# Performance work log

Hardware: AMD Instinct MI355X
Metric: run time of the kernel (lower is better)

## Reference

```python
import jax, jax.numpy as jnp
import numpy as np
import math

B, S, D, H, FF = 2, 2048, 1024, 16, 4096
E = D // H  # per-head dim = 64
LN_EPS = 1e-5


def _layernorm(x, g, b):
    m = jnp.mean(x, axis=-1, keepdims=True)
    v = jnp.var(x, axis=-1, keepdims=True)
    return (x - m) * jax.lax.rsqrt(v + LN_EPS) * g + b


def setup_inputs() -> dict:
    key = jax.random.key(0)
    ks = jax.random.split(key, 12)
    std = 0.02
    return {
        "inputs": jax.random.normal(ks[0], (B, S, D), dtype=jnp.float32),
        "ln1_g": jnp.ones((D,), jnp.float32),
        "ln1_b": jnp.zeros((D,), jnp.float32),
        # per-head q/k/v Linear(D, E) stacked along head axis: [H, D, E]
        "wq": jax.random.normal(ks[1], (H, D, E), jnp.float32) * std,
        "bq": jax.random.normal(ks[2], (H, E), jnp.float32) * std,
        "wk": jax.random.normal(ks[3], (H, D, E), jnp.float32) * std,
        "bk": jax.random.normal(ks[4], (H, E), jnp.float32) * std,
        "wv": jax.random.normal(ks[5], (H, D, E), jnp.float32) * std,
        "bv": jax.random.normal(ks[6], (H, E), jnp.float32) * std,
        "wo": jax.random.normal(ks[7], (D, D), jnp.float32) * std,
        "bo": jnp.zeros((D,), jnp.float32),
        "ln2_g": jnp.ones((D,), jnp.float32),
        "ln2_b": jnp.zeros((D,), jnp.float32),
        "w1": jax.random.normal(ks[8], (D, FF), jnp.float32) * std,
        "b1": jnp.zeros((FF,), jnp.float32),
        "w2": jax.random.normal(ks[9], (FF, D), jnp.float32) * std,
        "b2": jnp.zeros((D,), jnp.float32),
    }


def reference(inputs, ln1_g, ln1_b, wq, bq, wk, bk, wv, bv, wo, bo,
              ln2_g, ln2_b, w1, b1, w2, b2):
    d_model = inputs.shape[-1]
    scale = jnp.asarray(math.sqrt(d_model), inputs.dtype)  # NOTE: sqrt(d_model), not d_head

    x1 = _layernorm(inputs, ln1_g, ln1_b)
    # batched per-head projections (original uses H separate Linear layers)
    q = jnp.einsum('bsd,hde->bhse', x1, wq) + bq[None, :, None, :]
    k = jnp.einsum('bsd,hde->bhse', x1, wk) + bk[None, :, None, :]
    v = jnp.einsum('bsd,hde->bhse', x1, wv) + bv[None, :, None, :]

    scores = jnp.einsum('bhqe,bhke->bhqk', q, k) / scale
    # original: nn.Softmax(dim=1) on [B, S_q, S_k] -> softmax over the QUERY axis
    attn = jax.nn.softmax(scores, axis=2)
    a = jnp.einsum('bhqk,bhke->bhqe', attn, v)  # [B, H, S, E]

    # concat heads along feature dim (head 0 first)
    bsz, _, slen, _ = a.shape
    a = a.transpose(0, 2, 1, 3).reshape(bsz, slen, d_model)
    msa = a @ wo + bo

    inter = msa + inputs
    x2 = _layernorm(inter, ln2_g, ln2_b)
    mlp = jax.nn.gelu(x2 @ w1 + b1, approximate=False) @ w2 + b2
    return mlp + inter
```

## Files before the change

### kernel.cpp

```cpp
#include <hip/hip_runtime.h>
#include <hip/hip_bf16.h>

typedef unsigned short u16;
typedef __attribute__((ext_vector_type(8))) short short8;
typedef __attribute__((ext_vector_type(4))) float f32x4;
typedef __attribute__((ext_vector_type(4))) unsigned short us4;
typedef __attribute__((ext_vector_type(4))) float float4v;

#define DEV __device__ __forceinline__

DEV float b2f(u16 v){ return __uint_as_float(((unsigned)v)<<16); }
DEV u16 f2b(float f){
  unsigned u = __float_as_uint(f);
  u = u + 0x7FFFu + ((u>>16)&1u);
  return (u16)(u>>16);
}
DEV f32x4 mfma16(short8 a, short8 b, f32x4 c){
  return __builtin_amdgcn_mfma_f32_16x16x32_bf16(a, b, c, 0, 0, 0);
}
DEV void async16(const void* g, const void* l){
  __builtin_amdgcn_global_load_lds(
    (const __attribute__((address_space(1))) unsigned int*)(uintptr_t)g,
    (__attribute__((address_space(3))) unsigned int*)(unsigned int)(uintptr_t)l,
    16, 0, 0);
}

__global__ __launch_bounds__(256) void ln_k(const float* __restrict__ xin,
    const float* __restrict__ g, const float* __restrict__ bb, u16* __restrict__ y)
{
  const int row = blockIdx.x, t = threadIdx.x, l = t&63, w = t>>6;
  const float4v rr = *(const float4v*)(xin + (size_t)row*1024 + t*4);
  float v[4] = {rr[0], rr[1], rr[2], rr[3]};
  float s  = v[0]+v[1]+v[2]+v[3];
  float ss = v[0]*v[0]+v[1]*v[1]+v[2]*v[2]+v[3]*v[3];
#pragma unroll
  for (int off=32; off>=1; off>>=1){
    s  += __shfl_down(s,  off, 64);
    ss += __shfl_down(ss, off, 64);
  }
  __shared__ float rs[4], rq[4];
  if (l==0){ rs[w]=s; rq[w]=ss; }
  __syncthreads();
  const float S = rs[0]+rs[1]+rs[2]+rs[3];
  const float Q = rq[0]+rq[1]+rq[2]+rq[3];
  const float mean = S*(1.0f/1024.0f);
  const float var  = Q*(1.0f/1024.0f) - mean*mean;
  const float rstd = rsqrtf(var + 1e-5f);
  const float4v gg = *(const float4v*)(g  + t*4);
  const float4v bv = *(const float4v*)(bb + t*4);
  us4 o;
#pragma unroll
  for (int j=0;j<4;j++) o[j] = f2b((v[j]-mean)*rstd*gg[j] + bv[j]);
  *(us4*)(y + (size_t)row*1024 + t*4) = o;
}

__global__ void transpose_k(const float* __restrict__ src, u16* __restrict__ dst,
                            int ldsrc, int lddst)
{
  __shared__ u16 tile[32][33];
  const int tx = threadIdx.x & 31, ty = threadIdx.x >> 5;
  const int c0 = blockIdx.x*32, r0 = blockIdx.y*32;
#pragma unroll
  for (int i=0;i<32;i+=8) tile[ty+i][tx] = f2b(src[(size_t)(r0+ty+i)*ldsrc + c0+tx]);
  __syncthreads();
#pragma unroll
  for (int i=0;i<32;i+=8) dst[(size_t)(c0+ty+i)*lddst + r0+tx] = tile[tx][ty+i];
}

__global__ void pack_qkv_k(const float* __restrict__ wq, const float* __restrict__ wk,
                           const float* __restrict__ wv, u16* __restrict__ BT)
{
  __shared__ u16 tile[32][33];
  const int z = blockIdx.z, which = z>>4, h = z&15;
  const float* w = (which==0?wq:(which==1?wk:wv)) + (size_t)h*1024*64;
  u16* d = BT + (size_t)(which*1024 + h*64)*1024;
  const int tx = threadIdx.x & 31, ty = threadIdx.x >> 5;
  const int c0 = blockIdx.x*32, r0 = blockIdx.y*32;
#pragma unroll
  for (int i=0;i<32;i+=8) tile[ty+i][tx] = f2b(w[(size_t)(r0+ty+i)*64 + c0+tx]);
  __syncthreads();
#pragma unroll
  for (int i=0;i<32;i+=8) d[(size_t)(c0+ty+i)*1024 + r0+tx] = tile[tx][ty+i];
}

__global__ void pack_bias_k(const float* __restrict__ bq, const float* __restrict__ bk,
                            const float* __restrict__ bv, float* __restrict__ dst)
{
  const int t = blockIdx.x*256 + threadIdx.x;
  const float* s = (t < 1024) ? bq : (t < 2048 ? bk : bv);
  dst[t] = s[t & 1023];
}

__global__ __launch_bounds__(256) void inv_l(const float* __restrict__ L, float* __restrict__ invL)
{
  const int i = blockIdx.x*256 + threadIdx.x;
  invL[i] = 1.0f / (L[i] + L[i + 65536]);
}

template<int EPI>
__global__ __launch_bounds__(256) void gemm_bt(
    const u16* __restrict__ A, const u16* __restrict__ BT,
    const float* __restrict__ bias, const float* __restrict__ resf,
    u16* __restrict__ outb, float* __restrict__ outf,
    int K, int lda, int ldb, int ldc)
{
  __shared__ u16 Asm[128*32];
  __shared__ u16 Bsm[128*32];
  const int t = threadIdx.x, l = t&63, w = t>>6;
  const int bn = blockIdx.x, bm = blockIdx.y;
  const u16* gA = A  + (size_t)(bm*128 + (t>>2))*lda + (t&3)*8;
  const u16* gB = BT + (size_t)(bn*128 + (t>>2))*ldb + (t&3)*8;
  char* lA = (char*)Asm + t*16;
  char* lB = (char*)Bsm + t*16;
  const int wr = (w>>1)*64, wc = (w&1)*64;
  f32x4 acc[4][4] = {};
  for (int kt = 0; kt < K; kt += 32) {
    __syncthreads();
    async16(gA + kt,                    lA);
    async16(gA + kt + (size_t)64*lda,   lA + 4096);
    async16(gB + kt,                    lB);
    async16(gB + kt + (size_t)64*ldb,   lB + 4096);
    __syncthreads();
    short8 af[4], bf[4];
#pragma unroll
    for (int m=0;m<4;m++) af[m] = *(const short8*)&Asm[(wr + m*16 + (l&15))*32 + (l>>4)*8];
#pragma unroll
    for (int n=0;n<4;n++) bf[n] = *(const short8*)&Bsm[(wc + n*16 + (l&15))*32 + (l>>4)*8];
#pragma unroll
    for (int m=0;m<4;m++)
#pragma unroll
      for (int n=0;n<4;n++)
        acc[m][n] = mfma16(af[m], bf[n], acc[m][n]);
  }
  const int rowb = bm*128 + wr, colb = bn*128 + wc;
#pragma unroll
  for (int m=0;m<4;m++)
#pragma unroll
    for (int n=0;n<4;n++){
      const int col = colb + n*16 + (l&15);
      const float bv = bias[col];
#pragma unroll
      for (int j=0;j<4;j++){
        const int row = rowb + m*16 + (l>>4)*4 + j;
        float v = acc[m][n][j] + bv;
        const size_t idx = (size_t)row*ldc + col;
        if constexpr (EPI==0)      outb[idx] = f2b(v);
        else if constexpr (EPI==1) outf[idx] = v + resf[idx];
        else                       outb[idx] = f2b(0.5f*v*(1.0f + erff(v*0.70710678118654752f)));
      }
    }
}

template<int EPI>
__global__ __launch_bounds__(256) void gemm_bt64(
    const u16* __restrict__ A, const u16* __restrict__ BT,
    const float* __restrict__ bias, const float* __restrict__ resf,
    u16* __restrict__ outb, float* __restrict__ outf,
    int K, int lda, int ldb, int ldc)
{
  __shared__ u16 Asm[128*32];
  __shared__ u16 Bsm[64*32];
  const int t = threadIdx.x, l = t&63, w = t>>6;
  const int bn = blockIdx.x, bm = blockIdx.y;
  const u16* gA = A  + (size_t)(bm*128 + (t>>2))*lda + (t&3)*8;
  const u16* gB = BT + (size_t)(bn*64  + (t>>2))*ldb + (t&3)*8;
  char* lA = (char*)Asm + t*16;
  char* lB = (char*)Bsm + t*16;
  const int wr = w*32;
  f32x4 acc[2][4] = {};
  for (int kt = 0; kt < K; kt += 32) {
    __syncthreads();
    async16(gA + kt,                    lA);
    async16(gA + kt + (size_t)64*lda,   lA + 4096);
    async16(gB + kt,                    lB);
    __syncthreads();
    short8 af[2], bf[4];
#pragma unroll
    for (int m=0;m<2;m++) af[m] = *(const short8*)&Asm[(wr + m*16 + (l&15))*32 + (l>>4)*8];
#pragma unroll
    for (int n=0;n<4;n++) bf[n] = *(const short8*)&Bsm[(n*16 + (l&15))*32 + (l>>4)*8];
#pragma unroll
    for (int m=0;m<2;m++)
#pragma unroll
      for (int n=0;n<4;n++)
        acc[m][n] = mfma16(af[m], bf[n], acc[m][n]);
  }
  const int rowb = bm*128 + wr, colb = bn*64;
#pragma unroll
  for (int m=0;m<2;m++)
#pragma unroll
    for (int n=0;n<4;n++){
      const int col = colb + n*16 + (l&15);
      const float bv = bias[col];
#pragma unroll
      for (int j=0;j<4;j++){
        const int row = rowb + m*16 + (l>>4)*4 + j;
        float v = acc[m][n][j] + bv;
        const size_t idx = (size_t)row*ldc + col;
        if constexpr (EPI==0)      outb[idx] = f2b(v);
        else if constexpr (EPI==1) outf[idx] = v + resf[idx];
        else                       outb[idx] = f2b(0.5f*v*(1.0f + erff(v*0.70710678118654752f)));
      }
    }
}


__global__ __launch_bounds__(256) void attn_stats(const u16* __restrict__ QKV, float* __restrict__ L)
{
  const int g = blockIdx.x;
  const int xcd = g & 7, s_ = g >> 3;
  const int bh   = xcd*4 + (s_ & 3);
  const int kblk = (s_ >> 2) & 15;
  const int part = s_ >> 6;
  const int b = bh>>4, h = bh&15;
  const u16* Qb = QKV + (size_t)b*2048*3072 + h*64;
  const u16* Kb = Qb + 1024;
  __shared__ u16 Klds[128*64];
  __shared__ float red[4][128];
  const int t = threadIdx.x, l = t&63, w = t>>6;
#pragma unroll
  for (int i=0;i<8;i++){
    const int c = t + i*256, r = c>>4, ch = c&15;
    us4 v = *(const us4*)(Kb + (size_t)(kblk*128 + r)*3072 + ch*4);
    *(us4*)((char*)Klds + ((r*128 + ch*8) ^ ((r&7)<<4))) = v;
  }
  __syncthreads();
  short8 kf[8][2];
#pragma unroll
  for (int n=0;n<8;n++){
    const int r = n*16 + (l&15);
    const int sw = (r&7)<<4;
#pragma unroll
    for (int ks=0;ks<2;ks++)
      kf[n][ks] = *(const short8*)((char*)Klds + ((r*128 + ks*64 + (l>>4)*16) ^ sw));
  }
  float Lacc[8] = {0,0,0,0,0,0,0,0};
  short8 qf[2][2], qn[2][2];
  {
    const int qb = part*1024 + w*32;
#pragma unroll
    for (int m=0;m<2;m++)
#pragma unroll
      for (int ks=0;ks<2;ks++)
        qf[m][ks] = *(const short8*)(Qb + (size_t)(qb + m*16 + (l&15))*3072 + ks*32 + (l>>4)*8);
  }
  for (int qt = 0; qt < 8; qt++){
    if (qt < 7){
      const int qb = part*1024 + (qt+1)*128 + w*32;
#pragma unroll
      for (int m=0;m<2;m++)
#pragma unroll
        for (int ks=0;ks<2;ks++)
          qn[m][ks] = *(const short8*)(Qb + (size_t)(qb + m*16 + (l&15))*3072 + ks*32 + (l>>4)*8);
    }
#pragma unroll
    for (int m=0;m<2;m++)
#pragma unroll
      for (int n=0;n<8;n++){
        f32x4 s = {};
        s = mfma16(qf[m][0], kf[n][0], s);
        s = mfma16(qf[m][1], kf[n][1], s);
#pragma unroll
        for (int j=0;j<4;j++) Lacc[n] += __expf(s[j]*0.03125f);
      }
    if (qt < 7){
#pragma unroll
      for (int m=0;m<2;m++)
#pragma unroll
        for (int ks=0;ks<2;ks++) qf[m][ks] = qn[m][ks];
    }
  }
#pragma unroll
  for (int n=0;n<8;n++){
    Lacc[n] += __shfl_xor(Lacc[n], 16, 64);
    Lacc[n] += __shfl_xor(Lacc[n], 32, 64);
  }
  if (l < 16){
#pragma unroll
    for (int n=0;n<8;n++) red[w][n*16 + l] = Lacc[n];
  }
  __syncthreads();
  if (t < 128)
    L[(size_t)part*65536 + (size_t)bh*2048 + kblk*128 + t]
        = red[0][t]+red[1][t]+red[2][t]+red[3][t];
}

__global__ __launch_bounds__(256) void attn_pv(const u16* __restrict__ QKV,
    const float* __restrict__ invL, u16* __restrict__ Aout)
{
  const int g = blockIdx.x;
  const int xcd = g & 7, s_ = g >> 3;
  const int bh = xcd*4 + (s_ & 3);
  const int qblk = s_ >> 2;
  const int b = bh>>4, h = bh&15;
  const u16* Qb = QKV + (size_t)b*2048*3072 + h*64;
  const u16* Kb = Qb + 1024;
  const u16* Vb = Qb + 2048;
  const float* iL = invL + (size_t)bh*2048;
  __shared__ u16 Klds[64*64];
  __shared__ u16 VT[64*66];
  __shared__ u16 P[64*68];
  __shared__ float iLs[64];
  const int t = threadIdx.x, l = t&63, w = t>>6;
  short8 qf[2];
#pragma unroll
  for (int ks=0;ks<2;ks++)
    qf[ks] = *(const short8*)(Qb + (size_t)(qblk*64 + w*16 + (l&15))*3072 + ks*32 + (l>>4)*8);
  int rr[4], cc[4];
#pragma unroll
  for (int i=0;i<4;i++){ const int c = t + i*256; rr[i] = c>>4; cc[i] = c&15; }
  us4 kreg[4], vreg[4];
#pragma unroll
  for (int i=0;i<4;i++){
    kreg[i] = *(const us4*)(Kb + (size_t)rr[i]*3072 + cc[i]*4);
    vreg[i] = *(const us4*)(Vb + (size_t)rr[i]*3072 + cc[i]*4);
  }
  float ilreg = (t < 64) ? iL[t] : 0.0f;
  f32x4 acc[4] = {};
  for (int kt=0; kt<2048; kt+=64){
#pragma unroll
    for (int i=0;i<4;i++)
      *(us4*)((char*)Klds + ((rr[i]*128 + cc[i]*8) ^ ((rr[i]&7)<<4))) = kreg[i];
    if (t < 64) iLs[t] = ilreg;
    __syncthreads();
#pragma unroll
    for (int i=0;i<4;i++){
#pragma unroll
      for (int jj=0;jj<4;jj++) VT[(cc[i]*4+jj)*66 + rr[i]] = vreg[i][jj];
    }
    if (kt + 64 < 2048){
      const u16* Kn = Kb + (size_t)(kt+64)*3072;
      const u16* Vn = Vb + (size_t)(kt+64)*3072;
#pragma unroll
      for (int i=0;i<4;i++){
        kreg[i] = *(const us4*)(Kn + (size_t)rr[i]*3072 + cc[i]*4);
        vreg[i] = *(const us4*)(Vn + (size_t)rr[i]*3072 + cc[i]*4);
      }
      if (t < 64) ilreg = iL[kt + 64 + t];
    }
    float il[4];
#pragma unroll
    for (int n=0;n<4;n++) il[n] = iLs[n*16 + (l&15)];
#pragma unroll
    for (int n=0;n<4;n++){
      const int r = n*16 + (l&15);
      const int sw = (r&7)<<4;
      const short8 kf0 = *(const short8*)((char*)Klds + ((r*128 +      (l>>4)*16) ^ sw));
      const short8 kf1 = *(const short8*)((char*)Klds + ((r*128 + 64 + (l>>4)*16) ^ sw));
      f32x4 s = {};
      s = mfma16(qf[0], kf0, s);
      s = mfma16(qf[1], kf1, s);
      const int prow = w*16 + (l>>4)*4;
      const int pcol = n*16 + (l&15);
#pragma unroll
      for (int j=0;j<4;j++)
        P[(prow+j)*68 + pcol] = f2b(__expf(s[j]*0.03125f) * il[n]);
    }
    __syncthreads();
#pragma unroll
    for (int kk=0;kk<2;kk++){
      const short8 af = *(const short8*)&P[(w*16 + (l&15))*68 + kk*32 + (l>>4)*8];
#pragma unroll
      for (int n=0;n<4;n++){
        const short8 bf = *(const short8*)&VT[(n*16 + (l&15))*66 + kk*32 + (l>>4)*8];
        acc[n] = mfma16(af, bf, acc[n]);
      }
    }
  }
  const int rowb = b*2048 + qblk*64 + w*16;
  const int colb = h*64;
#pragma unroll
  for (int n=0;n<4;n++)
#pragma unroll
    for (int j=0;j<4;j++){
      const int row = rowb + (l>>4)*4 + j;
      const int col = colb + n*16 + (l&15);
      Aout[(size_t)row*1024 + col] = f2b(acc[n][j]);
    }
}

extern "C" void kernel_launch(void* const* d_in, const int* in_sizes, int n_in,
                              void* d_out, int out_size, void* d_ws, size_t ws_size,
                              hipStream_t stream)
{
  const float* x    = (const float*)d_in[0];
  const float* ln1g = (const float*)d_in[1];
  const float* ln1b = (const float*)d_in[2];
  const float* wq   = (const float*)d_in[3];
  const float* bq   = (const float*)d_in[4];
  const float* wk   = (const float*)d_in[5];
  const float* bk   = (const float*)d_in[6];
  const float* wv   = (const float*)d_in[7];
  const float* bv   = (const float*)d_in[8];
  const float* wo   = (const float*)d_in[9];
  const float* bo   = (const float*)d_in[10];
  const float* ln2g = (const float*)d_in[11];
  const float* ln2b = (const float*)d_in[12];
  const float* w1   = (const float*)d_in[13];
  const float* b1   = (const float*)d_in[14];
  const float* w2   = (const float*)d_in[15];
  const float* b2   = (const float*)d_in[16];
  float* out = (float*)d_out;

  char* ws = (char*)d_ws;
  u16*   x1      = (u16*)  (ws + 0);
  u16*   QKV     = (u16*)  (ws + 8388608);
  u16*   H1      = (u16*)  (ws + 8388608);
  float* Lbuf    = (float*)(ws + 41943040);
  u16*   Aout    = (u16*)  (ws + 42467328);
  u16*   packbuf = (u16*)  (ws + 50855936);
  float* inter   = (float*)(ws + 59244544);
  float* biasqkv = (float*)(ws + 76021760);
  float* invLb   = (float*)(ws + 76038144);
  u16*   x2 = x1;

  pack_bias_k<<<12, 256, 0, stream>>>(bq, bk, bv, biasqkv);

  ln_k<<<4096, 256, 0, stream>>>(x, ln1g, ln1b, x1);
  pack_qkv_k<<<dim3(2,32,48), 256, 0, stream>>>(wq, wk, wv, packbuf);
  gemm_bt<0><<<dim3(24,32), 256, 0, stream>>>(x1, packbuf, biasqkv,
      nullptr, QKV, nullptr, 1024, 1024, 1024, 3072);

  attn_stats<<<1024, 256, 0, stream>>>(QKV, Lbuf);
  inv_l<<<256, 256, 0, stream>>>(Lbuf, invLb);
  attn_pv  <<<1024, 256, 0, stream>>>(QKV, invLb, Aout);

  transpose_k<<<dim3(32,32), 256, 0, stream>>>(wo, packbuf, 1024, 1024);
  gemm_bt64<1><<<dim3(16,32), 256, 0, stream>>>(Aout, packbuf, bo,
      x, nullptr, inter, 1024, 1024, 1024, 1024);

  ln_k<<<4096, 256, 0, stream>>>(inter, ln2g, ln2b, x2);

  transpose_k<<<dim3(128,32), 256, 0, stream>>>(w1, packbuf, 4096, 1024);
  gemm_bt<2><<<dim3(32,32), 256, 0, stream>>>(x2, packbuf, b1,
      nullptr, H1, nullptr, 1024, 1024, 1024, 4096);

  transpose_k<<<dim3(32,128), 256, 0, stream>>>(w2, packbuf, 1024, 4096);
  gemm_bt64<1><<<dim3(16,32), 256, 0, stream>>>(H1, packbuf, b2,
      inter, nullptr, out, 4096, 4096, 4096, 1024);
}
```

Before: 476.9 us.

## Double-buffer GEMM LDS tiles with K=64 steps and XOR-swizzled layout

Replaces the two single-buffered GEMM kernels with one templated kernel. It double-buffers LDS so the next tile's global-to-LDS async loads overlap the current tile's MFMAs, doubles the K step to 64, and XOR-swizzles the LDS chunk layout to cut bank conflicts on fragment reads. The cost is twice the LDS per block (about 64KB for BN=128), which can reduce occupancy. There is also a reliance on the async loads finishing at the single barrier per iteration.

```diff
diff --git a/kernel.cpp b/kernel.cpp
--- a/kernel.cpp
+++ b/kernel.cpp
@@ -97,97 +97,81 @@
   invL[i] = 1.0f / (L[i] + L[i + 65536]);
 }
 
-template<int EPI>
-__global__ __launch_bounds__(256) void gemm_bt(
+template<int EPI, int BN>
+__global__ __launch_bounds__(256) void gemm2(
     const u16* __restrict__ A, const u16* __restrict__ BT,
     const float* __restrict__ bias, const float* __restrict__ resf,
     u16* __restrict__ outb, float* __restrict__ outf,
     int K, int lda, int ldb, int ldc)
 {
-  __shared__ u16 Asm[128*32];
-  __shared__ u16 Bsm[128*32];
+  constexpr int MF   = (BN==128) ? 4 : 2;
+  constexpr int BISS = BN/32;
+  __shared__ u16 smem[2][(128+BN)*64];
   const int t = threadIdx.x, l = t&63, w = t>>6;
   const int bn = blockIdx.x, bm = blockIdx.y;
-  const u16* gA = A  + (size_t)(bm*128 + (t>>2))*lda + (t&3)*8;
-  const u16* gB = BT + (size_t)(bn*128 + (t>>2))*ldb + (t&3)*8;
-  char* lA = (char*)Asm + t*16;
-  char* lB = (char*)Bsm + t*16;
-  const int wr = (w>>1)*64, wc = (w&1)*64;
-  f32x4 acc[4][4] = {};
-  for (int kt = 0; kt < K; kt += 32) {
+  const int wr = (BN==128) ? (w>>1)*64 : w*32;
+  const int wc = (BN==128) ? (w&1)*64  : 0;
+  const int srow = t>>3;
+  const int schunk = ((t&7) ^ (srow&7)) * 8;
+  const u16* gA = A  + (size_t)(bm*128 + srow)*lda + schunk;
+  const u16* gB = BT + (size_t)(bn*BN  + srow)*ldb + schunk;
+  char* ldsA0 = (char*)&smem[0][0];
+  char* ldsB0 = (char*)&smem[0][128*64];
+  char* ldsA1 = (char*)&smem[1][0];
+  char* ldsB1 = (char*)&smem[1][128*64];
+  int colx[2];
+#pragma unroll
+  for (int kk=0;kk<2;kk++) colx[kk] = (kk*64 + (l>>4)*16) ^ ((l&7)<<4);
+  int rowA[MF], rowB[4];
+#pragma unroll
+  for (int m=0;m<MF;m++) rowA[m] = (wr + m*16 + (l&15))*128;
+#pragma unroll
+  for (int n=0;n<4;n++)  rowB[n] = (wc + n*16 + (l&15))*128;
+
+#define STAGE(bufA, bufB, kt)                                            \
+  {                                                                      \
+    _Pragma("unroll")                                                    \
+    for (int i=0;i<4;i++)                                                \
+      async16(gA + (kt) + (size_t)i*32*lda, (bufA) + i*4096 + t*16);     \
+    _Pragma("unroll")                                                    \
+    for (int i=0;i<BISS;i++)                                             \
+      async16(gB + (kt) + (size_t)i*32*ldb, (bufB) + i*4096 + t*16);     \
+  }
+
+  f32x4 acc[MF][4] = {};
+  STAGE(ldsA0, ldsB0, 0);
+  __syncthreads();
+  const int nt = K >> 6;
+  int cur = 0;
+  for (int ti = 0; ti < nt; ++ti){
+    char* cA = cur ? ldsA1 : ldsA0;
+    char* cB = cur ? ldsB1 : ldsB0;
+    if (ti + 1 < nt){
+      char* pA = cur ? ldsA0 : ldsA1;
+      char* pB = cur ? ldsB0 : ldsB1;
+      STAGE(pA, pB, (ti+1)*64);
+    }
+#pragma unroll
+    for (int kk=0;kk<2;kk++){
+      short8 af[MF], bf[4];
+#pragma unroll
+      for (int m=0;m<MF;m++) af[m] = *(const short8*)(cA + rowA[m] + colx[kk]);
+#pragma unroll
+      for (int n=0;n<4;n++)  bf[n] = *(const short8*)(cB + rowB[n] + colx[kk]);
+#pragma unroll
+      for (int m=0;m<MF;m++)
+#pragma unroll
+        for (int n=0;n<4;n++)
+          acc[m][n] = mfma16(af[m], bf[n], acc[m][n]);
+    }
     __syncthreads();
-    async16(gA + kt,                    lA);
-    async16(gA + kt + (size_t)64*lda,   lA + 4096);
-    async16(gB + kt,                    lB);
-    async16(gB + kt + (size_t)64*ldb,   lB + 4096);
-    __syncthreads();
-    short8 af[4], bf[4];
-#pragma unroll
-    for (int m=0;m<4;m++) af[m] = *(const short8*)&Asm[(wr + m*16 + (l&15))*32 + (l>>4)*8];
-#pragma unroll
-    for (int n=0;n<4;n++) bf[n] = *(const short8*)&Bsm[(wc + n*16 + (l&15))*32 + (l>>4)*8];
-#pragma unroll
-    for (int m=0;m<4;m++)
-#pragma unroll
-      for (int n=0;n<4;n++)
-        acc[m][n] = mfma16(af[m], bf[n], acc[m][n]);
-  }
-  const int rowb = bm*128 + wr, colb = bn*128 + wc;
-#pragma unroll
-  for (int m=0;m<4;m++)
-#pragma unroll
-    for (int n=0;n<4;n++){
-      const int col = colb + n*16 + (l&15);
-      const float bv = bias[col];
-#pragma unroll
-      for (int j=0;j<4;j++){
-        const int row = rowb + m*16 + (l>>4)*4 + j;
-        float v = acc[m][n][j] + bv;
-        const size_t idx = (size_t)row*ldc + col;
-        if constexpr (EPI==0)      outb[idx] = f2b(v);
-        else if constexpr (EPI==1) outf[idx] = v + resf[idx];
-        else                       outb[idx] = f2b(0.5f*v*(1.0f + erff(v*0.70710678118654752f)));
-      }
-    }
-}
-
-template<int EPI>
-__global__ __launch_bounds__(256) void gemm_bt64(
-    const u16* __restrict__ A, const u16* __restrict__ BT,
-    const float* __restrict__ bias, const float* __restrict__ resf,
-    u16* __restrict__ outb, float* __restrict__ outf,
-    int K, int lda, int ldb, int ldc)
-{
-  __shared__ u16 Asm[128*32];
-  __shared__ u16 Bsm[64*32];
-  const int t = threadIdx.x, l = t&63, w = t>>6;
-  const int bn = blockIdx.x, bm = blockIdx.y;
-  const u16* gA = A  + (size_t)(bm*128 + (t>>2))*lda + (t&3)*8;
-  const u16* gB = BT + (size_t)(bn*64  + (t>>2))*ldb + (t&3)*8;
-  char* lA = (char*)Asm + t*16;
-  char* lB = (char*)Bsm + t*16;
-  const int wr = w*32;
-  f32x4 acc[2][4] = {};
-  for (int kt = 0; kt < K; kt += 32) {
-    __syncthreads();
-    async16(gA + kt,                    lA);
-    async16(gA + kt + (size_t)64*lda,   lA + 4096);
-    async16(gB + kt,                    lB);
-    __syncthreads();
-    short8 af[2], bf[4];
-#pragma unroll
-    for (int m=0;m<2;m++) af[m] = *(const short8*)&Asm[(wr + m*16 + (l&15))*32 + (l>>4)*8];
-#pragma unroll
-    for (int n=0;n<4;n++) bf[n] = *(const short8*)&Bsm[(n*16 + (l&15))*32 + (l>>4)*8];
-#pragma unroll
-    for (int m=0;m<2;m++)
-#pragma unroll
-      for (int n=0;n<4;n++)
-        acc[m][n] = mfma16(af[m], bf[n], acc[m][n]);
-  }
-  const int rowb = bm*128 + wr, colb = bn*64;
-#pragma unroll
-  for (int m=0;m<2;m++)
+    cur ^= 1;
+  }
+#undef STAGE
+
+  const int rowb = bm*128 + wr, colb = bn*BN + wc;
+#pragma unroll
+  for (int m=0;m<MF;m++)
 #pragma unroll
     for (int n=0;n<4;n++){
       const int col = colb + n*16 + (l&15);
@@ -418,7 +402,7 @@
 
   ln_k<<<4096, 256, 0, stream>>>(x, ln1g, ln1b, x1);
   pack_qkv_k<<<dim3(2,32,48), 256, 0, stream>>>(wq, wk, wv, packbuf);
-  gemm_bt<0><<<dim3(24,32), 256, 0, stream>>>(x1, packbuf, biasqkv,
+  gemm2<0,128><<<dim3(24,32), 256, 0, stream>>>(x1, packbuf, biasqkv,
       nullptr, QKV, nullptr, 1024, 1024, 1024, 3072);
 
   attn_stats<<<1024, 256, 0, stream>>>(QKV, Lbuf);
@@ -426,16 +410,16 @@
   attn_pv  <<<1024, 256, 0, stream>>>(QKV, invLb, Aout);
 
   transpose_k<<<dim3(32,32), 256, 0, stream>>>(wo, packbuf, 1024, 1024);
-  gemm_bt64<1><<<dim3(16,32), 256, 0, stream>>>(Aout, packbuf, bo,
+  gemm2<1,64><<<dim3(16,32), 256, 0, stream>>>(Aout, packbuf, bo,
       x, nullptr, inter, 1024, 1024, 1024, 1024);
 
   ln_k<<<4096, 256, 0, stream>>>(inter, ln2g, ln2b, x2);
 
   transpose_k<<<dim3(128,32), 256, 0, stream>>>(w1, packbuf, 4096, 1024);
-  gemm_bt<2><<<dim3(32,32), 256, 0, stream>>>(x2, packbuf, b1,
+  gemm2<2,128><<<dim3(32,32), 256, 0, stream>>>(x2, packbuf, b1,
       nullptr, H1, nullptr, 1024, 1024, 1024, 4096);
 
   transpose_k<<<dim3(32,128), 256, 0, stream>>>(w2, packbuf, 1024, 4096);
-  gemm_bt64<1><<<dim3(16,32), 256, 0, stream>>>(H1, packbuf, b2,
+  gemm2<1,64><<<dim3(16,32), 256, 0, stream>>>(H1, packbuf, b2,
       inter, nullptr, out, 4096, 4096, 4096, 1024);
 }
```

Result: faster. 434.7 us (-8.9%).
